# Kernel tuning notes

Hardware: AMD Instinct MI355X
Metric: run time of the kernel (lower is better)

## Reference

```python
import jax, jax.numpy as jnp
import numpy as np

K = 20  # hard-coded in Codebook.forward


def _renorm(x):
    # x / ||x||_2 along dim 1, matching torch renorm()
    return x / jnp.linalg.norm(x, axis=1, keepdims=True)


def setup_inputs() -> dict:
    key = jax.random.key(0)
    ks = jax.random.split(key, 6)
    B, N, D = 2048, 50000, 128
    z_rot = jax.random.normal(ks[0], (B, D), dtype=jnp.float32)
    z_trans = jax.random.normal(ks[1], (B, D), dtype=jnp.float32)
    # rotation codebook entries are pre-renormed in create_codetensors
    z_rot_book = _renorm(jax.random.normal(ks[2], (N, D), dtype=jnp.float32))
    z_trans_book = jax.random.normal(ks[3], (N, D), dtype=jnp.float32)
    rot_book = jax.random.uniform(ks[4], (N, 1), dtype=jnp.float32) * 360.0
    trans_book = jax.random.normal(ks[5], (N, 3), dtype=jnp.float32)
    return {
        "z_rot": z_rot,
        "z_trans": z_trans,
        "z_rot_book": z_rot_book,
        "z_trans_book": z_trans_book,
        "rot_book": rot_book,
        "trans_book": trans_book,
    }


def reference(z_rot, z_trans, z_rot_book, z_trans_book, rot_book, trans_book):
    # --- get_nearest_cosine ---
    zr = _renorm(z_rot)                                   # [B, D]
    cos = jnp.einsum("bd,nd->bn", zr, z_rot_book)        # [B, N]
    vals_cos, ind_cos = jax.lax.top_k(cos, K)             # [B, K]
    labels_rot = rot_book[ind_cos]                        # [B, K, 1]

    # --- get_nearest_euclidean ---
    # -(||z - b||^2) = -(||z||^2 - 2 z.b + ||b||^2); avoids the [B,N,D]
    # broadcasted intermediate the torch code materializes (same math).
    zq = jnp.sum(z_trans * z_trans, axis=1, keepdims=True)          # [B, 1]
    bq = jnp.sum(z_trans_book * z_trans_book, axis=1)               # [N]
    m2 = 2.0 * jnp.einsum("bd,nd->bn", z_trans, z_trans_book) - zq - bq[None, :]
    vals_euc, ind_euc = jax.lax.top_k(m2, K)              # [B, K]
    labels_trans = trans_book[ind_euc]                    # [B, K, 3]

    return vals_cos, ind_cos, labels_rot, vals_euc, ind_euc, labels_trans
```

## Files before the change

kernel.cpp:

```cpp
#include <hip/hip_runtime.h>
#include <cfloat>
#include <climits>
#include <math.h>

#define BB 2048
#define NN 50000
#define DD 128
#define KK 20

#define NSLICE 16
#define NSL 3125
#define NTILE 98
#define TAILV 21
#define LK 8
#define SLC 16
#define CAND 256
#define K1W 4

#define O_VC 0
#define O_IC 40960
#define O_LR 81920
#define O_VE 122880
#define O_IE 163840
#define O_LT 204800

#define WS_BBF   0
#define WS_BQ2   25690112
#define WS_CAND  25890112

typedef short v8s __attribute__((ext_vector_type(8)));
typedef float v16f __attribute__((ext_vector_type(16)));

union U4V8 { uint4 u; v8s v; };

__device__ __forceinline__ unsigned int bf16rne(float f) {
    unsigned int x = __float_as_uint(f);
    return (x + 0x7FFFu + ((x >> 16) & 1u)) >> 16;
}
__device__ __forceinline__ unsigned int sortkey(float s) {
    unsigned int b = __float_as_uint(s);
    return b ^ ((unsigned int)((int)b >> 31) | 0x80000000u);
}

__device__ __forceinline__ void ce(unsigned int &a, unsigned int &b) {
    unsigned int lo = min(a, b);
    unsigned int hi = max(a, b);
    a = lo; b = hi;
}
__device__ __forceinline__ void sort8(unsigned int* k) {
    ce(k[0],k[1]); ce(k[2],k[3]); ce(k[4],k[5]); ce(k[6],k[7]);
    ce(k[0],k[2]); ce(k[1],k[3]); ce(k[4],k[6]); ce(k[5],k[7]);
    ce(k[1],k[2]); ce(k[5],k[6]);
    ce(k[0],k[4]); ce(k[1],k[5]); ce(k[2],k[6]); ce(k[3],k[7]);
    ce(k[2],k[4]); ce(k[3],k[5]);
    ce(k[1],k[2]); ce(k[3],k[4]); ce(k[5],k[6]);
}
__device__ __forceinline__ void merge8(unsigned int (&run)[LK], const unsigned int* s) {
    unsigned int m[8];
    #pragma unroll
    for (int i = 0; i < 8; i++) m[i] = max(run[i], s[7 - i]);
    ce(m[0],m[4]); ce(m[1],m[5]); ce(m[2],m[6]); ce(m[3],m[7]);
    ce(m[0],m[2]); ce(m[1],m[3]); ce(m[4],m[6]); ce(m[5],m[7]);
    ce(m[0],m[1]); ce(m[2],m[3]); ce(m[4],m[5]); ce(m[6],m[7]);
    #pragma unroll
    for (int i = 0; i < 8; i++) run[i] = m[i];
}

__global__ __launch_bounds__(256) void k_cvt2(const float* __restrict__ bR,
                                              const float* __restrict__ bT,
                                              unsigned int* __restrict__ Bbf,
                                              unsigned int* __restrict__ bq2)
{
    const int tile  = blockIdx.x;
    const int slice = blockIdx.y;
    const int task  = blockIdx.z;
    const int t = threadIdx.x;
    const float* __restrict__ src = task ? bT : bR;
    const float sc = task ? 2.f : 1.f;

    __shared__ float ps[4][64];

    unsigned int* tb = Bbf + (((size_t)(task * NSLICE + slice) * NTILE + tile) << 11);

    float partial = 0.f;
    #pragma unroll
    for (int half = 0; half < 2; half++) {
        const int x = t + half * 256;
        const int c = x & 31, hh = (x >> 5) & 1, q = x >> 6;
        const int es = slice * NSL + min(tile * 32 + c, NSL - 1);
        const float* p = src + (size_t)es * DD + q * 16 + hh * 8;
        float4 u0 = *reinterpret_cast<const float4*>(p);
        float4 u1 = *reinterpret_cast<const float4*>(p + 4);
        partial += u0.x * u0.x + u0.y * u0.y + u0.z * u0.z + u0.w * u0.w
                 + u1.x * u1.x + u1.y * u1.y + u1.z * u1.z + u1.w * u1.w;
        uint4 o;
        o.x = bf16rne(u0.x * sc) | (bf16rne(u0.y * sc) << 16);
        o.y = bf16rne(u0.z * sc) | (bf16rne(u0.w * sc) << 16);
        o.z = bf16rne(u1.x * sc) | (bf16rne(u1.y * sc) << 16);
        o.w = bf16rne(u1.z * sc) | (bf16rne(u1.w * sc) << 16);
        *reinterpret_cast<uint4*>(tb + (q << 8) + hh * 128 + c * 4) = o;
    }

    if (task) {
        ps[t >> 6][t & 63] = partial;
        __syncthreads();
        if (t < 32) {
            float sq = 0.f;
            #pragma unroll
            for (int w2 = 0; w2 < 4; w2++) sq += ps[w2][t] + ps[w2][t + 32];
            unsigned int hi = bf16rne(sq);
            float fhi = __uint_as_float(hi << 16);
            unsigned int lo = bf16rne(sq - fhi);
            const int e = slice * NSL + min(tile * 32 + t, NSL - 1);
            bq2[e] = (hi ^ 0x8000u) | ((lo ^ 0x8000u) << 16);
        }
    }
}

__global__ __launch_bounds__(256, 4) void k1_sel(
    const float* __restrict__ zR, const float* __restrict__ zT,
    const unsigned int* __restrict__ Bbf,
    const unsigned int* __restrict__ bq2,
    uint4* __restrict__ candU)
{
    const int slice = blockIdx.x;
    const int rg    = blockIdx.y;
    const int task  = blockIdx.z;
    const int w     = threadIdx.x >> 6;
    const int lane  = threadIdx.x & 63;
    const int col   = lane & 31;
    const int h     = lane >> 5;

    __shared__ unsigned int smk[K1W - 1][64][LK + 1];

    const float* zp = (task ? zT : zR) + (size_t)(rg * 32 + col) * DD;
    v8s zf[9];
    #pragma unroll
    for (int q = 0; q < 8; q++) {
        float4 u0 = *reinterpret_cast<const float4*>(zp + q * 16 + h * 8);
        float4 u1 = *reinterpret_cast<const float4*>(zp + q * 16 + h * 8 + 4);
        U4V8 c;
        c.u.x = bf16rne(u0.x) | (bf16rne(u0.y) << 16);
        c.u.y = bf16rne(u0.z) | (bf16rne(u0.w) << 16);
        c.u.z = bf16rne(u1.x) | (bf16rne(u1.y) << 16);
        c.u.w = bf16rne(u1.z) | (bf16rne(u1.w) << 16);
        zf[q] = c.v;
    }
    {
        U4V8 c; c.u = make_uint4(h == 0 ? 0x3F803F80u : 0u, 0u, 0u, 0u);
        zf[8] = c.v;
    }

    unsigned int run[LK];
    #pragma unroll
    for (int u = 0; u < LK; u++) run[u] = 0u;

    const int nbase0 = slice * NSL;
    const unsigned int* bp = Bbf + ((size_t)(task * NSLICE + slice) * NTILE << 11) + lane * 4;

#define TILE_BODY(TILE, TAIL)                                                          \
    {                                                                                  \
        const unsigned int* tb = bp + ((size_t)(TILE) << 11);                          \
        v16f acc = {0.f,0.f,0.f,0.f, 0.f,0.f,0.f,0.f,                                  \
                    0.f,0.f,0.f,0.f, 0.f,0.f,0.f,0.f};                                 \
        _Pragma("unroll")                                                              \
        for (int q = 0; q < 8; q++) {                                                  \
            U4V8 a; a.u = *reinterpret_cast<const uint4*>(tb + (q << 8));              \
            acc = __builtin_amdgcn_mfma_f32_32x32x16_bf16(a.v, zf[q], acc, 0, 0, 0);   \
        }                                                                              \
        if (task) {                                                                    \
            int e = nbase0 + (TILE) * 32 + col;                                        \
            if (TAIL) e = min(e, nbase0 + NSL - 1);                                    \
            unsigned int bqp = bq2[e];                                                 \
            U4V8 a; a.u = make_uint4(h == 0 ? bqp : 0u, 0u, 0u, 0u);                   \
            acc = __builtin_amdgcn_mfma_f32_32x32x16_bf16(a.v, zf[8], acc, 0, 0, 0);   \
        }                                                                              \
        const int nb = nbase0 + (TILE) * 32 + 4 * h;                                   \
        unsigned int kk[16];                                                           \
        _Pragma("unroll")                                                              \
        for (int r = 0; r < 16; r++) {                                                 \
            const int pat = (r & 3) + 8 * (r >> 2);                                    \
            const int n = nb + pat;                                                    \
            unsigned int k = (sortkey(acc[r]) & 0xFFFF0000u) | (unsigned int)n;        \
            if (TAIL && (pat + 4 * h >= TAILV)) k = 0u;                                \
            kk[r] = k;                                                                 \
        }                                                                              \
        sort8(&kk[0]); sort8(&kk[8]);                                                  \
        merge8(run, &kk[0]); merge8(run, &kk[8]);                                      \
    }

    int tile = w;
    for (; tile < NTILE - 1; tile += K1W) TILE_BODY(tile, 0)
    if (tile == NTILE - 1) TILE_BODY(tile, 1)
#undef TILE_BODY

    if (w > 0) {
        #pragma unroll
        for (int u = 0; u < LK; u++) smk[w - 1][lane][u] = run[u];
    }
    __syncthreads();
    if (w == 0) {
        #pragma unroll
        for (int v = 0; v < K1W - 1; v++) {
            unsigned int s[LK];
            #pragma unroll
            for (int u = 0; u < LK; u++) s[u] = smk[v][lane][u];
            merge8(run, s);
        }

        uint4 o;
        o.x = (run[0] & 0xFFFFu) | ((run[1] & 0xFFFFu) << 16);
        o.y = (run[2] & 0xFFFFu) | ((run[3] & 0xFFFFu) << 16);
        o.z = (run[4] & 0xFFFFu) | ((run[5] & 0xFFFFu) << 16);
        o.w = (run[6] & 0xFFFFu) | ((run[7] & 0xFFFFu) << 16);
        const int row = rg * 32 + col;
        candU[((size_t)(task * BB + row) * NSLICE + slice) * 2 + h] = o;
    }
}

__global__ __launch_bounds__(256) void k2_final(
    const float* __restrict__ Zr, const float* __restrict__ Zt,
    const float* __restrict__ Br, const float* __restrict__ Bt,
    const float* __restrict__ rotB, const float* __restrict__ transB,
    const unsigned short* __restrict__ candU16,
    float* __restrict__ out)
{
    const int row = blockIdx.x;
    const int task = blockIdx.y;
    const int t = threadIdx.x;
    const float* __restrict__ Z  = task ? Zt : Zr;
    const float* __restrict__ Bk = task ? Bt : Br;

    __shared__ __align__(16) float zrow[DD];
    __shared__ int sel[CAND];
    __shared__ double dsum[CAND];
    __shared__ double sval[KK];
    __shared__ int sidx[KK];
    __shared__ float sv[CAND];

    if (t < DD) zrow[t] = Z[(size_t)row * DD + t];
    sel[t] = (int)candU16[((size_t)task * BB + row) * CAND + t];
    __syncthreads();

    if (task == 0) {
        #pragma unroll
        for (int it = 0; it < 8; it++) {
            const int idx = t + it * 256;
            const int cnd = idx >> 3, part = idx & 7;
            const int n = sel[cnd];
            const float* brow = Bk + (size_t)n * DD + part * 16;
            double dp = 0.0;
            #pragma unroll
            for (int q = 0; q < 4; q++) {
                float4 b4 = *reinterpret_cast<const float4*>(brow + q * 4);
                const int k = part * 16 + q * 4;
                dp += (double)zrow[k + 0] * (double)b4.x + (double)zrow[k + 1] * (double)b4.y
                    + (double)zrow[k + 2] * (double)b4.z + (double)zrow[k + 3] * (double)b4.w;
            }
            dp += __shfl_xor(dp, 1, 64);
            dp += __shfl_xor(dp, 2, 64);
            dp += __shfl_xor(dp, 4, 64);
            if ((t & 7) == 0) dsum[cnd] = dp;
        }
        __syncthreads();

        if (t < 64) {
            double zq = (double)zrow[t] * (double)zrow[t]
                      + (double)zrow[t + 64] * (double)zrow[t + 64];
            #pragma unroll
            for (int m = 1; m < 64; m <<= 1) zq += __shfl_xor(zq, m, 64);

            double s[4]; int ix[4];
            #pragma unroll
            for (int j = 0; j < 4; j++) {
                const int c = t + 64 * j;
                s[j] = dsum[c]; ix[j] = sel[c];
            }

            for (int rd = 0; rd < KK; rd++) {
                double bs = s[0]; int bn = ix[0];
                #pragma unroll
                for (int j = 1; j < 4; j++)
                    if (s[j] > bs || (s[j] == bs && ix[j] < bn)) { bs = s[j]; bn = ix[j]; }
                #pragma unroll
                for (int m = 1; m < 64; m <<= 1) {
                    double os = __shfl_xor(bs, m, 64);
                    int on = __shfl_xor(bn, m, 64);
                    if (os > bs || (os == bs && on < bn)) { bs = os; bn = on; }
                }
                #pragma unroll
                for (int j = 0; j < 4; j++) if (ix[j] == bn) s[j] = -DBL_MAX;
                if (t == 0) { sval[rd] = bs; sidx[rd] = bn; }
            }
            if (t == 0) dsum[0] = zq;
        }
        __syncthreads();

        if (t < KK) {
            const double zq = dsum[0];
            const int n = sidx[t];
            const int o = row * KK + t;
            out[O_VC + o] = (float)(sval[t] / sqrt(zq));
            out[O_IC + o] = (float)n;
            out[O_LR + o] = rotB[n];
        }
    } else {
        {
            const int n = sel[t];
            const float* brow = Bk + (size_t)n * DD;
            float L[4], r[8], q[8];
            #pragma unroll
            for (int u = 0; u < 4; u++) L[u] = 0.f;
            #pragma unroll
            for (int u = 0; u < 8; u++) { r[u] = 0.f; q[u] = 0.f; }
            #pragma unroll
            for (int c4 = 0; c4 < 32; c4++) {
                float4 b4 = *reinterpret_cast<const float4*>(brow + c4 * 4);
                float4 z4 = *reinterpret_cast<const float4*>(&zrow[c4 * 4]);
                const int m8 = (c4 & 1) * 4;
                L[0] = __fadd_rn(L[0], __fmul_rn(z4.x, b4.x));
                L[1] = __fadd_rn(L[1], __fmul_rn(z4.y, b4.y));
                L[2] = __fadd_rn(L[2], __fmul_rn(z4.z, b4.z));
                L[3] = __fadd_rn(L[3], __fmul_rn(z4.w, b4.w));
                r[m8 + 0] = __fadd_rn(r[m8 + 0], __fmul_rn(b4.x, b4.x));
                r[m8 + 1] = __fadd_rn(r[m8 + 1], __fmul_rn(b4.y, b4.y));
                r[m8 + 2] = __fadd_rn(r[m8 + 2], __fmul_rn(b4.z, b4.z));
                r[m8 + 3] = __fadd_rn(r[m8 + 3], __fmul_rn(b4.w, b4.w));
                q[m8 + 0] = __fadd_rn(q[m8 + 0], __fmul_rn(z4.x, z4.x));
                q[m8 + 1] = __fadd_rn(q[m8 + 1], __fmul_rn(z4.y, z4.y));
                q[m8 + 2] = __fadd_rn(q[m8 + 2], __fmul_rn(z4.z, z4.z));
                q[m8 + 3] = __fadd_rn(q[m8 + 3], __fmul_rn(z4.w, z4.w));
            }
            const float dot = __fadd_rn(__fadd_rn(L[0], L[2]), __fadd_rn(L[1], L[3]));
            const float bqv = __fadd_rn(__fadd_rn(__fadd_rn(r[0], r[1]), __fadd_rn(r[2], r[3])),
                                        __fadd_rn(__fadd_rn(r[4], r[5]), __fadd_rn(r[6], r[7])));
            const float zqv = __fadd_rn(__fadd_rn(__fadd_rn(q[0], q[1]), __fadd_rn(q[2], q[3])),
                                        __fadd_rn(__fadd_rn(q[4], q[5]), __fadd_rn(q[6], q[7])));
            sv[t] = __fsub_rn(__fsub_rn(__fmul_rn(2.0f, dot), zqv), bqv);
        }
        __syncthreads();

        if (t < 64) {
            float s[4]; int ix[4];
            #pragma unroll
            for (int j = 0; j < 4; j++) { s[j] = sv[t + 64 * j]; ix[j] = sel[t + 64 * j]; }

            for (int rd = 0; rd < KK; rd++) {
                float bs = s[0]; int bn = ix[0];
                #pragma unroll
                for (int j = 1; j < 4; j++)
                    if (s[j] > bs || (s[j] == bs && ix[j] < bn)) { bs = s[j]; bn = ix[j]; }
                #pragma unroll
                for (int m = 1; m < 64; m <<= 1) {
                    float os = __shfl_xor(bs, m, 64);
                    int on = __shfl_xor(bn, m, 64);
                    if (os > bs || (os == bs && on < bn)) { bs = os; bn = on; }
                }
                #pragma unroll
                for (int j = 0; j < 4; j++) if (ix[j] == bn) s[j] = -FLT_MAX;
                if (t == 0) {
                    const int o = row * KK + rd;
                    out[O_VE + o] = bs;
                    out[O_IE + o] = (float)bn;
                    const int o3 = O_LT + o * 3;
                    out[o3 + 0] = transB[bn * 3 + 0];
                    out[o3 + 1] = transB[bn * 3 + 1];
                    out[o3 + 2] = transB[bn * 3 + 2];
                }
            }
        }
    }
}

extern "C" void kernel_launch(void* const* d_in, const int* in_sizes, int n_in,
                              void* d_out, int out_size, void* d_ws, size_t ws_size,
                              hipStream_t stream) {
    const float* zR = (const float*)d_in[0];
    const float* zT = (const float*)d_in[1];
    const float* bR = (const float*)d_in[2];
    const float* bT = (const float*)d_in[3];
    const float* rotB = (const float*)d_in[4];
    const float* transB = (const float*)d_in[5];
    float* out = (float*)d_out;

    char* ws = (char*)d_ws;
    unsigned int* Bbf = (unsigned int*)(ws + WS_BBF);
    unsigned int* bq2 = (unsigned int*)(ws + WS_BQ2);
    uint4* candU = (uint4*)(ws + WS_CAND);

    k_cvt2<<<dim3(NTILE, NSLICE, 2), 256, 0, stream>>>(bR, bT, Bbf, bq2);
    k1_sel<<<dim3(NSLICE, 64, 2), 256, 0, stream>>>(zR, zT, Bbf, bq2, candU);
    k2_final<<<dim3(BB, 2), 256, 0, stream>>>(zR, zT, bR, bT, rotB, transB,
                                              (const unsigned short*)candU, out);
}
```

Before: 369.1 us.

## Stage z operand in LDS, use med3 insertion top-8, raise occupancy

Only wave 0 now converts the query rows to bf16, stores them in shared memory, and every wave reads them per tile instead of keeping nine vector registers each. The per-tile sort8+merge8 network is replaced by a 16-step insertion into the running top-8 built on v_med3_u32, which costs about 8 ops per key. Launch bounds move from 4 to 8 blocks per CU, relying on the lower register use to double occupancy. The trade is extra LDS reads per MFMA, a barrier at the start, and a longer dependent chain of med3 ops per key.

```diff
diff --git a/kernel.cpp b/kernel.cpp
--- a/kernel.cpp
+++ b/kernel.cpp
@@ -41,19 +41,20 @@
     unsigned int b = __float_as_uint(s);
     return b ^ ((unsigned int)((int)b >> 31) | 0x80000000u);
 }
-
+__device__ __forceinline__ unsigned int med3u(unsigned int a, unsigned int b, unsigned int c) {
+    unsigned int d;
+    asm("v_med3_u32 %0, %1, %2, %3" : "=v"(d) : "v"(a), "v"(b), "v"(c));
+    return d;
+}
+__device__ __forceinline__ void ins8(unsigned int (&run)[LK], unsigned int k) {
+    #pragma unroll
+    for (int u = 0; u < LK - 1; u++) run[u] = med3u(k, run[u], run[u + 1]);
+    run[LK - 1] = max(k, run[LK - 1]);
+}
 __device__ __forceinline__ void ce(unsigned int &a, unsigned int &b) {
     unsigned int lo = min(a, b);
     unsigned int hi = max(a, b);
     a = lo; b = hi;
-}
-__device__ __forceinline__ void sort8(unsigned int* k) {
-    ce(k[0],k[1]); ce(k[2],k[3]); ce(k[4],k[5]); ce(k[6],k[7]);
-    ce(k[0],k[2]); ce(k[1],k[3]); ce(k[4],k[6]); ce(k[5],k[7]);
-    ce(k[1],k[2]); ce(k[5],k[6]);
-    ce(k[0],k[4]); ce(k[1],k[5]); ce(k[2],k[6]); ce(k[3],k[7]);
-    ce(k[2],k[4]); ce(k[3],k[5]);
-    ce(k[1],k[2]); ce(k[3],k[4]); ce(k[5],k[6]);
 }
 __device__ __forceinline__ void merge8(unsigned int (&run)[LK], const unsigned int* s) {
     unsigned int m[8];
@@ -117,7 +118,7 @@
     }
 }
 
-__global__ __launch_bounds__(256, 4) void k1_sel(
+__global__ __launch_bounds__(256, 8) void k1_sel(
     const float* __restrict__ zR, const float* __restrict__ zT,
     const unsigned int* __restrict__ Bbf,
     const unsigned int* __restrict__ bq2,
@@ -131,25 +132,25 @@
     const int col   = lane & 31;
     const int h     = lane >> 5;
 
+    __shared__ uint4 zs[8][64];
     __shared__ unsigned int smk[K1W - 1][64][LK + 1];
 
-    const float* zp = (task ? zT : zR) + (size_t)(rg * 32 + col) * DD;
-    v8s zf[9];
-    #pragma unroll
-    for (int q = 0; q < 8; q++) {
-        float4 u0 = *reinterpret_cast<const float4*>(zp + q * 16 + h * 8);
-        float4 u1 = *reinterpret_cast<const float4*>(zp + q * 16 + h * 8 + 4);
-        U4V8 c;
-        c.u.x = bf16rne(u0.x) | (bf16rne(u0.y) << 16);
-        c.u.y = bf16rne(u0.z) | (bf16rne(u0.w) << 16);
-        c.u.z = bf16rne(u1.x) | (bf16rne(u1.y) << 16);
-        c.u.w = bf16rne(u1.z) | (bf16rne(u1.w) << 16);
-        zf[q] = c.v;
-    }
-    {
-        U4V8 c; c.u = make_uint4(h == 0 ? 0x3F803F80u : 0u, 0u, 0u, 0u);
-        zf[8] = c.v;
-    }
+    if (w == 0) {
+        const float* zp = (task ? zT : zR) + (size_t)(rg * 32 + col) * DD;
+        #pragma unroll
+        for (int q = 0; q < 8; q++) {
+            float4 u0 = *reinterpret_cast<const float4*>(zp + q * 16 + h * 8);
+            float4 u1 = *reinterpret_cast<const float4*>(zp + q * 16 + h * 8 + 4);
+            uint4 c;
+            c.x = bf16rne(u0.x) | (bf16rne(u0.y) << 16);
+            c.y = bf16rne(u0.z) | (bf16rne(u0.w) << 16);
+            c.z = bf16rne(u1.x) | (bf16rne(u1.y) << 16);
+            c.w = bf16rne(u1.z) | (bf16rne(u1.w) << 16);
+            zs[q][lane] = c;
+        }
+    }
+    U4V8 zf8; zf8.u = make_uint4(h == 0 ? 0x3F803F80u : 0u, 0u, 0u, 0u);
+    __syncthreads();
 
     unsigned int run[LK];
     #pragma unroll
@@ -160,33 +161,32 @@
 
 #define TILE_BODY(TILE, TAIL)                                                          \
     {                                                                                  \
+        asm volatile("" ::: "memory");   \
         const unsigned int* tb = bp + ((size_t)(TILE) << 11);                          \
         v16f acc = {0.f,0.f,0.f,0.f, 0.f,0.f,0.f,0.f,                                  \
                     0.f,0.f,0.f,0.f, 0.f,0.f,0.f,0.f};                                 \
         _Pragma("unroll")                                                              \
         for (int q = 0; q < 8; q++) {                                                  \
             U4V8 a; a.u = *reinterpret_cast<const uint4*>(tb + (q << 8));              \
-            acc = __builtin_amdgcn_mfma_f32_32x32x16_bf16(a.v, zf[q], acc, 0, 0, 0);   \
+            U4V8 z; z.u = zs[q][lane];                                                 \
+            acc = __builtin_amdgcn_mfma_f32_32x32x16_bf16(a.v, z.v, acc, 0, 0, 0);     \
         }                                                                              \
         if (task) {                                                                    \
             int e = nbase0 + (TILE) * 32 + col;                                        \
             if (TAIL) e = min(e, nbase0 + NSL - 1);                                    \
             unsigned int bqp = bq2[e];                                                 \
             U4V8 a; a.u = make_uint4(h == 0 ? bqp : 0u, 0u, 0u, 0u);                   \
-            acc = __builtin_amdgcn_mfma_f32_32x32x16_bf16(a.v, zf[8], acc, 0, 0, 0);   \
+            acc = __builtin_amdgcn_mfma_f32_32x32x16_bf16(a.v, zf8.v, acc, 0, 0, 0);   \
         }                                                                              \
         const int nb = nbase0 + (TILE) * 32 + 4 * h;                                   \
-        unsigned int kk[16];                                                           \
         _Pragma("unroll")                                                              \
         for (int r = 0; r < 16; r++) {                                                 \
             const int pat = (r & 3) + 8 * (r >> 2);                                    \
             const int n = nb + pat;                                                    \
             unsigned int k = (sortkey(acc[r]) & 0xFFFF0000u) | (unsigned int)n;        \
             if (TAIL && (pat + 4 * h >= TAILV)) k = 0u;                                \
-            kk[r] = k;                                                                 \
+            ins8(run, k);                                                              \
         }                                                                              \
-        sort8(&kk[0]); sort8(&kk[8]);                                                  \
-        merge8(run, &kk[0]); merge8(run, &kk[8]);                                      \
     }
 
     int tile = w;
```

Result: faster. 343.8 us (-6.9%).
